# Optimization experiments

Measured on AMD Instinct MI355X. Metric: run time of the kernel, lower is better.

## Reference

```python
import jax, jax.numpy as jnp
import numpy as np
from jax import lax

INPUT_SIZE = 16
RESERVOIR_SIZE = 1024
OUTPUT_SIZE = 16
SPECTRAL_RADIUS = 0.9
SPARSITY = 0.1
BATCH = 1024
SEQ_LEN = 4096


def setup_inputs() -> dict:
    key = jax.random.key(0)
    k_x, k_win, k_w, k_mask, k_wo, k_b = jax.random.split(key, 6)
    x = jax.random.normal(k_x, (BATCH, SEQ_LEN, INPUT_SIZE), dtype=jnp.float32)
    Win = jax.random.normal(k_win, (RESERVOIR_SIZE, INPUT_SIZE), dtype=jnp.float32)
    W = jax.random.normal(k_w, (RESERVOIR_SIZE, RESERVOIR_SIZE), dtype=jnp.float32)
    # spectral-radius rescaling (done once at init in the torch module)
    eig = np.linalg.eigvals(np.asarray(W))
    W = W * (SPECTRAL_RADIUS / np.max(np.abs(eig))).astype(np.float32)
    # sparsify with Bernoulli(sparsity) mask
    mask = (jax.random.uniform(k_mask, (RESERVOIR_SIZE, RESERVOIR_SIZE)) < SPARSITY).astype(jnp.float32)
    W = W * mask
    Wout_w = jax.random.normal(k_wo, (OUTPUT_SIZE, RESERVOIR_SIZE), dtype=jnp.float32) / np.sqrt(RESERVOIR_SIZE).astype(np.float32)
    Wout_b = jax.random.normal(k_b, (OUTPUT_SIZE,), dtype=jnp.float32) * 0.01
    return {"x": x, "Win": Win, "W": W, "Wout_w": Wout_w, "Wout_b": Wout_b}


def reference(x, Win, W, Wout_w, Wout_b):
    batch = x.shape[0]
    h0 = jnp.zeros((batch, W.shape[0]), dtype=x.dtype)

    def step(h, x_t):
        h = jnp.tanh(x_t @ Win.T + h @ W.T)
        return h, None

    # scan over time: x_time is [seq_len, batch, input_size]
    x_time = jnp.swapaxes(x, 0, 1)
    h_final, _ = lax.scan(step, h0, x_time)
    y = h_final @ Wout_w.T + Wout_b  # [batch, output_size]
    return y
```

## Files before the change

kernel.cpp:

```cpp
#include <hip/hip_runtime.h>

#define RS 1024
#define SL 4096
#define NB 1024
#define NI 16
#define RGRP 32
#define NGRP 32
#define WPG 8

typedef short s8v __attribute__((ext_vector_type(8)));
typedef float f16v __attribute__((ext_vector_type(16)));
typedef unsigned int u4v __attribute__((ext_vector_type(4)));

#define WAIT_VM(N) do { asm volatile("s_waitcnt vmcnt(" #N ")" ::: "memory"); \
                        __builtin_amdgcn_sched_barrier(0); } while (0)

static __device__ __forceinline__ unsigned short f2bf(float f) {
  unsigned u = __float_as_uint(f);
  u += 0x7fffu + ((u >> 16) & 1u);
  return (unsigned short)(u >> 16);
}
static __device__ __forceinline__ float bf2f(unsigned short b) {
  return __uint_as_float(((unsigned)b) << 16);
}
static __device__ __forceinline__ float fast_tanh(float a) {
  float e = __expf(2.0f * a);
  return 1.0f - 2.0f / (e + 1.0f);
}

static __device__ __forceinline__ u4v ld_llc_b128(const void* p) {
  u4v d;
  asm volatile("global_load_dwordx4 %0, %1, off sc0 sc1"
               : "=v"(d) : "v"(p) : "memory");
  return d;
}
static __device__ __forceinline__ void st_llc_b128(void* p, u4v d) {
  asm volatile("global_store_dwordx4 %0, %1, off sc0 sc1"
               : : "v"(p), "v"(d) : "memory");
}

__global__ __launch_bounds__(256) void prep_kernel(
    const float* __restrict__ W, unsigned short* __restrict__ wbf,
    uint4* __restrict__ hA4, int* __restrict__ flags) {
  int idx = blockIdx.x * 256 + threadIdx.x;
  if (idx < RS * RS) wbf[idx] = f2bf(W[idx]);
  if (idx < (NB * RS) / 8) hA4[idx] = make_uint4(0u, 0u, 0u, 0u);
  if (idx < NGRP * 64) flags[idx] = 0;
}

__global__ __launch_bounds__(256, 1) void esn_kernel(
    const float* __restrict__ x, const float* __restrict__ Win,
    const unsigned short* __restrict__ wbf,
    unsigned short* __restrict__ hA, unsigned short* __restrict__ hB,
    int* __restrict__ flags) {
  extern __shared__ char smem[];
  char* psm = smem;
  char* ctile = smem + 65536;

  const int bid = blockIdx.x;
  const int g = bid & 31;
  const int j = bid >> 5;
  const int tid = threadIdx.x;
  const int w = tid >> 6;
  const int lane = tid & 63;
  const int l31 = lane & 31;
  const int hi = lane >> 5;

  const int n0 = j * 128 + w * 32;
  const int m0 = g * RGRP;

  s8v bw[4][16];
#pragma unroll
  for (int idx = 0; idx < 4; idx++) {
    const int c = (w + idx) & 3;
    const unsigned short* wp =
        wbf + (size_t)(j * 128 + c * 32 + l31) * RS + w * 256 + hi * 8;
#pragma unroll
    for (int kk = 0; kk < 16; kk++) bw[idx][kk] = *(const s8v*)(wp + kk * 16);
  }

  union U8 { s8v v; unsigned short u[8]; };
  U8 whi, wlo;
  {
    const float* p = Win + (n0 + l31) * NI + hi * 8;
#pragma unroll
    for (int i = 0; i < 8; i++) {
      float f = p[i];
      unsigned short h16 = f2bf(f);
      whi.u[i] = h16;
      wlo.u[i] = f2bf(f - bf2f(h16));
    }
  }

  int* flag = flags + g * 64;
  const float* xrow = x + (size_t)(m0 + l31) * SL * NI + hi * 8;
  const size_t ab_off = (((size_t)(32 * w + hi) * NB) + m0 + l31) << 4;
  char* wct = ctile + w * 2048;
  int dead = 0;

  for (int t = 0; t < SL; t++) {
    const char* hsrc = (const char*)((t & 1) ? hB : hA);
    char* hdst = (char*)((t & 1) ? hA : hB);

    float4 xa = *(const float4*)(xrow + (size_t)t * NI);
    float4 xb = *(const float4*)(xrow + (size_t)t * NI + 4);

    if (t > 0) {
      if (tid == 0 && !dead) {
        const int target = t * WPG;
        int spins = 0;
        while (__hip_atomic_load(flag, __ATOMIC_RELAXED, __HIP_MEMORY_SCOPE_AGENT) < target) {
          __builtin_amdgcn_s_sleep(8);
          if (++spins > (1 << 16)) { dead = 1; break; }
        }
      }
      __syncthreads();
    }

    U8 xhi, xlo;
    {
      float xf[8] = {xa.x, xa.y, xa.z, xa.w, xb.x, xb.y, xb.z, xb.w};
#pragma unroll
      for (int i = 0; i < 8; i++) {
        unsigned short h16 = f2bf(xf[i]);
        xhi.u[i] = h16;
        xlo.u[i] = f2bf(xf[i] - bf2f(h16));
      }
    }
    __builtin_amdgcn_sched_barrier(0);

    u4v al[16];
#pragma unroll
    for (int kk = 0; kk < 16; kk++)
      al[kk] = ld_llc_b128(hsrc + ab_off + (size_t)kk * (2 * NB * 16));

    f16v acc[4];
    {
      f16v z = {};
      z = __builtin_amdgcn_mfma_f32_32x32x16_bf16(xhi.v, whi.v, z, 0, 0, 0);
      z = __builtin_amdgcn_mfma_f32_32x32x16_bf16(xlo.v, whi.v, z, 0, 0, 0);
      acc[0] = __builtin_amdgcn_mfma_f32_32x32x16_bf16(xhi.v, wlo.v, z, 0, 0, 0);
      f16v zz = {};
      acc[1] = zz; acc[2] = zz; acc[3] = zz;
    }

#define KBLK(K0)                                                            \
    _Pragma("unroll")                                                       \
    for (int kk = K0; kk < K0 + 4; kk++) {                                  \
      union AU { u4v u; s8v s; } au; au.u = al[kk];                         \
      _Pragma("unroll")                                                     \
      for (int idx = 0; idx < 4; idx++)                                     \
        acc[idx] = __builtin_amdgcn_mfma_f32_32x32x16_bf16(au.s, bw[idx][kk], acc[idx], 0, 0, 0); \
    }
    WAIT_VM(12); KBLK(0)
    WAIT_VM(8);  KBLK(4)
    WAIT_VM(4);  KBLK(8)
    WAIT_VM(0);  KBLK(12)
#undef KBLK

#pragma unroll
    for (int idx = 1; idx < 4; idx++) {
      const int c = (w + idx) & 3;
      char* slot = psm + (((c << 2) | w) << 12) + (size_t)l31 * 4;
#pragma unroll
      for (int r = 0; r < 16; r++)
        *(float*)(slot + (hi * 16 + r) * 128) = acc[idx][r];
    }
    __syncthreads();

    f16v own = acc[0];
#pragma unroll
    for (int idx = 1; idx < 4; idx++) {
      const int wp = (w + idx) & 3;
      const char* slot = psm + (((w << 2) | wp) << 12) + (size_t)l31 * 4;
#pragma unroll
      for (int r = 0; r < 16; r++)
        own[r] += *(const float*)(slot + (hi * 16 + r) * 128);
    }

#pragma unroll
    for (int r = 0; r < 16; r++) {
      const int row = (r & 3) + 8 * (r >> 2) + 4 * hi;
      *(unsigned short*)(wct + row * 64 + l31 * 2) = f2bf(fast_tanh(own[r]));
    }
    asm volatile("s_waitcnt lgkmcnt(0)" ::: "memory");
    __builtin_amdgcn_sched_barrier(0);
    {
      const int row = lane >> 1, c = lane & 1;
      u4v v0 = *(const u4v*)(wct + row * 64 + c * 16);
      u4v v1 = *(const u4v*)(wct + row * 64 + c * 16 + 32);
      char* g0 = hdst + ((((size_t)(n0 >> 3) + c) * NB + m0 + row) << 4);
      char* g1 = hdst + ((((size_t)(n0 >> 3) + c + 2) * NB + m0 + row) << 4);
      st_llc_b128(g0, v0);
      st_llc_b128(g1, v1);
    }
    WAIT_VM(0);
    __syncthreads();
    if (tid == 0)
      __hip_atomic_fetch_add(flag, 1, __ATOMIC_RELAXED, __HIP_MEMORY_SCOPE_AGENT);
  }
}

__global__ __launch_bounds__(256) void yout_kernel(
    const unsigned short* __restrict__ h, const float* __restrict__ Wout,
    const float* __restrict__ bias, float* __restrict__ y) {
  const int tid = threadIdx.x;
  const int b = (blockIdx.x << 4) + (tid >> 4);
  const int o = tid & 15;
  const float* wr = Wout + (o << 10);
  float s = 0.0f;
  for (int k8 = 0; k8 < RS / 8; k8++) {
    const unsigned short* hc = h + (((size_t)k8 * NB + b) << 3);
#pragma unroll
    for (int i = 0; i < 8; i++) s += bf2f(hc[i]) * wr[k8 * 8 + i];
  }
  y[(b << 4) + o] = s + bias[o];
}

extern "C" void kernel_launch(void* const* d_in, const int* in_sizes, int n_in,
                              void* d_out, int out_size, void* d_ws, size_t ws_size,
                              hipStream_t stream) {
  const float* x = (const float*)d_in[0];
  const float* Win = (const float*)d_in[1];
  const float* W = (const float*)d_in[2];
  const float* Wout = (const float*)d_in[3];
  const float* bias = (const float*)d_in[4];
  float* y = (float*)d_out;

  char* ws = (char*)d_ws;
  unsigned short* hA = (unsigned short*)ws;
  unsigned short* hB = (unsigned short*)(ws + (1 << 21));
  unsigned short* wbf = (unsigned short*)(ws + (2 << 21));
  int* flags = (int*)(ws + 3 * (size_t)(1 << 21));

  (void)hipFuncSetAttribute((const void*)esn_kernel,
                            hipFuncAttributeMaxDynamicSharedMemorySize, 73728);

  prep_kernel<<<4096, 256, 0, stream>>>(W, wbf, (uint4*)hA, flags);
  esn_kernel<<<NGRP * WPG, 256, 73728, stream>>>(x, Win, wbf, hA, hB, flags);
  yout_kernel<<<64, 256, 0, stream>>>(hA, Wout, bias, y);
}
```

Measured before the change: 17.76 ms.

## Replace per-group atomic counter barrier with per-wave flags polled per dependency

```diff
diff --git a/kernel.cpp b/kernel.cpp
--- a/kernel.cpp
+++ b/kernel.cpp
@@ -38,6 +38,16 @@
   asm volatile("global_store_dwordx4 %0, %1, off sc0 sc1"
                : : "v"(p), "v"(d) : "memory");
 }
+static __device__ __forceinline__ void st_llc_b32(void* p, int d) {
+  asm volatile("global_store_dword %0, %1, off sc0 sc1"
+               : : "v"(p), "v"(d) : "memory");
+}
+static __device__ __forceinline__ void ld_flags8(const void* p, u4v& a, u4v& b) {
+  asm volatile("global_load_dwordx4 %0, %2, off sc0 sc1\n\t"
+               "global_load_dwordx4 %1, %2, off offset:16 sc0 sc1\n\t"
+               "s_waitcnt vmcnt(0)"
+               : "=v"(a), "=v"(b) : "v"(p) : "memory");
+}
 
 __global__ __launch_bounds__(256) void prep_kernel(
     const float* __restrict__ W, unsigned short* __restrict__ wbf,
@@ -45,7 +55,7 @@
   int idx = blockIdx.x * 256 + threadIdx.x;
   if (idx < RS * RS) wbf[idx] = f2bf(W[idx]);
   if (idx < (NB * RS) / 8) hA4[idx] = make_uint4(0u, 0u, 0u, 0u);
-  if (idx < NGRP * 64) flags[idx] = 0;
+  if (idx < 4096) flags[idx] = 0;
 }
 
 __global__ __launch_bounds__(256, 1) void esn_kernel(
@@ -92,7 +102,9 @@
     }
   }
 
-  int* flag = flags + g * 64;
+  int* gflags = flags + g * 32;
+  int* myflag = gflags + 4 * j + w;
+  const int* pollp = gflags + 8 * w;
   const float* xrow = x + (size_t)(m0 + l31) * SL * NI + hi * 8;
   const size_t ab_off = (((size_t)(32 * w + hi) * NB) + m0 + l31) << 4;
   char* wct = ctile + w * 2048;
@@ -105,17 +117,23 @@
     float4 xa = *(const float4*)(xrow + (size_t)t * NI);
     float4 xb = *(const float4*)(xrow + (size_t)t * NI + 4);
 
-    if (t > 0) {
-      if (tid == 0 && !dead) {
-        const int target = t * WPG;
-        int spins = 0;
-        while (__hip_atomic_load(flag, __ATOMIC_RELAXED, __HIP_MEMORY_SCOPE_AGENT) < target) {
-          __builtin_amdgcn_s_sleep(8);
-          if (++spins > (1 << 16)) { dead = 1; break; }
-        }
+    if (!dead) {
+      int spins = 0;
+      for (;;) {
+        u4v f0, f1;
+        ld_flags8(pollp, f0, f1);
+        int m01 = min((int)f0.x, (int)f0.y), m23 = min((int)f0.z, (int)f0.w);
+        int m45 = min((int)f1.x, (int)f1.y), m67 = min((int)f1.z, (int)f1.w);
+        if (min(min(m01, m23), min(m45, m67)) >= t) break;
+        __builtin_amdgcn_s_sleep(1);
+        if (++spins > (1 << 12)) { dead = 1; break; }
       }
-      __syncthreads();
-    }
+    }
+
+    u4v al[16];
+#pragma unroll
+    for (int kk = 0; kk < 16; kk++)
+      al[kk] = ld_llc_b128(hsrc + ab_off + (size_t)kk * (2 * NB * 16));
 
     U8 xhi, xlo;
     {
@@ -127,12 +145,6 @@
         xlo.u[i] = f2bf(xf[i] - bf2f(h16));
       }
     }
-    __builtin_amdgcn_sched_barrier(0);
-
-    u4v al[16];
-#pragma unroll
-    for (int kk = 0; kk < 16; kk++)
-      al[kk] = ld_llc_b128(hsrc + ab_off + (size_t)kk * (2 * NB * 16));
 
     f16v acc[4];
     {
@@ -195,9 +207,8 @@
       st_llc_b128(g1, v1);
     }
     WAIT_VM(0);
+    if (lane == 0) st_llc_b32(myflag, t + 1);
     __syncthreads();
-    if (tid == 0)
-      __hip_atomic_fetch_add(flag, 1, __ATOMIC_RELAXED, __HIP_MEMORY_SCOPE_AGENT);
   }
 }
 
```

Measured after the change: 18.52 ms. 4.3% more time.

## Replace atomic flag barrier with parity bits embedded in bf16 hidden state

Applied to the files above, without the earlier changes.

```diff
diff --git a/kernel.cpp b/kernel.cpp
--- a/kernel.cpp
+++ b/kernel.cpp
@@ -12,8 +12,8 @@
 typedef float f16v __attribute__((ext_vector_type(16)));
 typedef unsigned int u4v __attribute__((ext_vector_type(4)));
 
-#define WAIT_VM(N) do { asm volatile("s_waitcnt vmcnt(" #N ")" ::: "memory"); \
-                        __builtin_amdgcn_sched_barrier(0); } while (0)
+#define WAIT_VM0 do { asm volatile("s_waitcnt vmcnt(0)" ::: "memory"); \
+                      __builtin_amdgcn_sched_barrier(0); } while (0)
 
 static __device__ __forceinline__ unsigned short f2bf(float f) {
   unsigned u = __float_as_uint(f);
@@ -41,18 +41,19 @@
 
 __global__ __launch_bounds__(256) void prep_kernel(
     const float* __restrict__ W, unsigned short* __restrict__ wbf,
-    uint4* __restrict__ hA4, int* __restrict__ flags) {
+    uint4* __restrict__ h0q, uint4* __restrict__ h1q) {
   int idx = blockIdx.x * 256 + threadIdx.x;
   if (idx < RS * RS) wbf[idx] = f2bf(W[idx]);
-  if (idx < (NB * RS) / 8) hA4[idx] = make_uint4(0u, 0u, 0u, 0u);
-  if (idx < NGRP * 64) flags[idx] = 0;
+  if (idx < (NB * RS) / 8) {
+    h0q[idx] = make_uint4(0u, 0u, 0u, 0u);
+    h1q[idx] = make_uint4(0x00010000u, 0x00010000u, 0x00010000u, 0x00010000u);
+  }
 }
 
 __global__ __launch_bounds__(256, 1) void esn_kernel(
     const float* __restrict__ x, const float* __restrict__ Win,
     const unsigned short* __restrict__ wbf,
-    unsigned short* __restrict__ hA, unsigned short* __restrict__ hB,
-    int* __restrict__ flags) {
+    unsigned short* __restrict__ hA, unsigned short* __restrict__ hB) {
   extern __shared__ char smem[];
   char* psm = smem;
   char* ctile = smem + 65536;
@@ -92,29 +93,51 @@
     }
   }
 
-  int* flag = flags + g * 64;
   const float* xrow = x + (size_t)(m0 + l31) * SL * NI + hi * 8;
   const size_t ab_off = (((size_t)(32 * w + hi) * NB) + m0 + l31) << 4;
   char* wct = ctile + w * 2048;
+  const unsigned oddm = (unsigned)(l31 & 1);
   int dead = 0;
+
+  u4v al[16];
+#pragma unroll
+  for (int kk = 0; kk < 16; kk++)
+    al[kk] = ld_llc_b128((const char*)hA + ab_off + (size_t)kk * (2 * NB * 16));
+  float4 xa = *(const float4*)(xrow);
+  float4 xb = *(const float4*)(xrow + 4);
 
   for (int t = 0; t < SL; t++) {
     const char* hsrc = (const char*)((t & 1) ? hB : hA);
     char* hdst = (char*)((t & 1) ? hA : hB);
 
-    float4 xa = *(const float4*)(xrow + (size_t)t * NI);
-    float4 xb = *(const float4*)(xrow + (size_t)t * NI + 4);
-
-    if (t > 0) {
-      if (tid == 0 && !dead) {
-        const int target = t * WPG;
-        int spins = 0;
-        while (__hip_atomic_load(flag, __ATOMIC_RELAXED, __HIP_MEMORY_SCOPE_AGENT) < target) {
-          __builtin_amdgcn_s_sleep(8);
-          if (++spins > (1 << 16)) { dead = 1; break; }
+    if (!dead) {
+      int spins = 0;
+      const unsigned want = (unsigned)((t >> 1) & 1);
+      for (;;) {
+        WAIT_VM0;
+        unsigned red;
+        if (want) {
+          red = 0xFFFFFFFFu;
+#pragma unroll
+          for (int kk = 0; kk < 16; kk++)
+            red &= al[kk].x & al[kk].y & al[kk].z & al[kk].w;
+          red = (red >> 16) & 1u;
+        } else {
+          red = 0u;
+#pragma unroll
+          for (int kk = 0; kk < 16; kk++)
+            red |= al[kk].x | al[kk].y | al[kk].z | al[kk].w;
+          red = ((red >> 16) & 1u) ^ 1u;
         }
+        if (__all((int)red)) break;
+        if (++spins > (1 << 12)) { dead = 1; break; }
+        __builtin_amdgcn_s_sleep(1);
+#pragma unroll
+        for (int kk = 0; kk < 16; kk++)
+          al[kk] = ld_llc_b128(hsrc + ab_off + (size_t)kk * (2 * NB * 16));
       }
-      __syncthreads();
+    } else {
+      WAIT_VM0;
     }
 
     U8 xhi, xlo;
@@ -127,12 +150,6 @@
         xlo.u[i] = f2bf(xf[i] - bf2f(h16));
       }
     }
-    __builtin_amdgcn_sched_barrier(0);
-
-    u4v al[16];
-#pragma unroll
-    for (int kk = 0; kk < 16; kk++)
-      al[kk] = ld_llc_b128(hsrc + ab_off + (size_t)kk * (2 * NB * 16));
 
     f16v acc[4];
     {
@@ -144,19 +161,13 @@
       acc[1] = zz; acc[2] = zz; acc[3] = zz;
     }
 
-#define KBLK(K0)                                                            \
-    _Pragma("unroll")                                                       \
-    for (int kk = K0; kk < K0 + 4; kk++) {                                  \
-      union AU { u4v u; s8v s; } au; au.u = al[kk];                         \
-      _Pragma("unroll")                                                     \
-      for (int idx = 0; idx < 4; idx++)                                     \
-        acc[idx] = __builtin_amdgcn_mfma_f32_32x32x16_bf16(au.s, bw[idx][kk], acc[idx], 0, 0, 0); \
-    }
-    WAIT_VM(12); KBLK(0)
-    WAIT_VM(8);  KBLK(4)
-    WAIT_VM(4);  KBLK(8)
-    WAIT_VM(0);  KBLK(12)
-#undef KBLK
+#pragma unroll
+    for (int kk = 0; kk < 16; kk++) {
+      union AU { u4v u; s8v s; } au; au.u = al[kk];
+#pragma unroll
+      for (int idx = 0; idx < 4; idx++)
+        acc[idx] = __builtin_amdgcn_mfma_f32_32x32x16_bf16(au.s, bw[idx][kk], acc[idx], 0, 0, 0);
+    }
 
 #pragma unroll
     for (int idx = 1; idx < 4; idx++) {
@@ -178,10 +189,13 @@
         own[r] += *(const float*)(slot + (hi * 16 + r) * 128);
     }
 
+    const unsigned taun = (unsigned)(((t + 1) >> 1) & 1);
 #pragma unroll
     for (int r = 0; r < 16; r++) {
       const int row = (r & 3) + 8 * (r >> 2) + 4 * hi;
-      *(unsigned short*)(wct + row * 64 + l31 * 2) = f2bf(fast_tanh(own[r]));
+      unsigned short hv = f2bf(fast_tanh(own[r]));
+      hv = (unsigned short)(((unsigned)hv & ~oddm) | (taun & oddm));
+      *(unsigned short*)(wct + row * 64 + l31 * 2) = hv;
     }
     asm volatile("s_waitcnt lgkmcnt(0)" ::: "memory");
     __builtin_amdgcn_sched_barrier(0);
@@ -194,10 +208,16 @@
       st_llc_b128(g0, v0);
       st_llc_b128(g1, v1);
     }
-    WAIT_VM(0);
+
+#pragma unroll
+    for (int kk = 0; kk < 16; kk++)
+      al[kk] = ld_llc_b128(hdst + ab_off + (size_t)kk * (2 * NB * 16));
+    {
+      const size_t xo = (size_t)((t + 1 < SL) ? t + 1 : 0) * NI;
+      xa = *(const float4*)(xrow + xo);
+      xb = *(const float4*)(xrow + xo + 4);
+    }
     __syncthreads();
-    if (tid == 0)
-      __hip_atomic_fetch_add(flag, 1, __ATOMIC_RELAXED, __HIP_MEMORY_SCOPE_AGENT);
   }
 }
 
@@ -231,12 +251,11 @@
   unsigned short* hA = (unsigned short*)ws;
   unsigned short* hB = (unsigned short*)(ws + (1 << 21));
   unsigned short* wbf = (unsigned short*)(ws + (2 << 21));
-  int* flags = (int*)(ws + 3 * (size_t)(1 << 21));
 
   (void)hipFuncSetAttribute((const void*)esn_kernel,
                             hipFuncAttributeMaxDynamicSharedMemorySize, 73728);
 
-  prep_kernel<<<4096, 256, 0, stream>>>(W, wbf, (uint4*)hA, flags);
-  esn_kernel<<<NGRP * WPG, 256, 73728, stream>>>(x, Win, wbf, hA, hB, flags);
+  prep_kernel<<<4096, 256, 0, stream>>>(W, wbf, (uint4*)hA, (uint4*)hB);
+  esn_kernel<<<NGRP * WPG, 256, 73728, stream>>>(x, Win, wbf, hA, hB);
   yout_kernel<<<64, 256, 0, stream>>>(hA, Wout, bias, y);
 }
```

After: 24.99 ms. 40.7% more time.
